# Performance work log

Hardware: AMD Instinct MI355X
Metric: run time of the kernel (lower is better)

## Reference

```python
import jax, jax.numpy as jnp
import numpy as np

H = 512      # hidden_size
N = 8        # num_heads (each head has full H dims in this module)
B, T = 4, 1024
LN_EPS = 1e-5


def _layernorm(x, gamma, beta):
    mu = jnp.mean(x, axis=-1, keepdims=True)
    var = jnp.mean(jnp.square(x - mu), axis=-1, keepdims=True)
    return (x - mu) * jax.lax.rsqrt(var + LN_EPS) * gamma + beta


def setup_inputs() -> dict:
    key = jax.random.key(0)
    ks = jax.random.split(key, 8)
    s = 0.02
    return {
        "x":   jax.random.normal(ks[0], (B, T, H), dtype=jnp.float32),
        "Wq":  jax.random.normal(ks[1], (H, N * H), dtype=jnp.float32) * s,
        "Wk":  jax.random.normal(ks[2], (H, N * H), dtype=jnp.float32) * s,
        "Wv":  jax.random.normal(ks[3], (H, N * H), dtype=jnp.float32) * s,
        "Wo":  jax.random.normal(ks[4], (N * H, H), dtype=jnp.float32) * s,
        "g1":  jnp.ones((H,), jnp.float32),
        "beta1": jnp.zeros((H,), jnp.float32),
        "Wf1": jax.random.normal(ks[5], (H, 4 * H), dtype=jnp.float32) * s,
        "bf1": jnp.zeros((4 * H,), jnp.float32),
        "Wf2": jax.random.normal(ks[6], (4 * H, H), dtype=jnp.float32) * s,
        "bf2": jnp.zeros((H,), jnp.float32),
        "g2":  jnp.ones((H,), jnp.float32),
        "beta2": jnp.zeros((H,), jnp.float32),
    }


def reference(x, Wq, Wk, Wv, Wo, g1, beta1, Wf1, bf1, Wf2, bf2, g2, beta2):
    b, t, h = x.shape
    n = Wq.shape[1] // h
    # torch .view(B, N, T, H) on a contiguous (B, T, N*H) tensor is a raw
    # row-major reshape (NOT a transpose) -> identical to jnp.reshape.
    Q = (x @ Wq).reshape(b, n, t, h)
    K = (x @ Wk).reshape(b, n, t, h)
    V = (x @ Wv).reshape(b, n, t, h)
    # 'bath,bahT->batT' with K.transpose(2,3) == standard Q @ K^T per (b,a)
    logits = jnp.einsum('bath,baTh->batT', Q, K)
    attn = jax.nn.softmax(logits / (h ** 0.5), axis=-1)
    # repeated 't' in one operand takes the DIAGONAL of attn (torch semantics,
    # matched by numpy/jax einsum): h[b,a,t,:] = attn[b,a,t,t] * V[b,a,t,:]
    hh = jnp.einsum('batt,bath->bath', attn, V)
    hh = hh.reshape(b, t, n * h) @ Wo
    hh = _layernorm(x + hh, g1, beta1)
    ff = jax.nn.relu(hh @ Wf1 + bf1) @ Wf2 + bf2
    return _layernorm(hh + ff, g2, beta2)
```

## Files before the change

### kernel.cpp

```cpp
#include <hip/hip_runtime.h>
#include <stdint.h>


#define LN_EPS 1e-5f

typedef __attribute__((ext_vector_type(8))) short short8;
typedef __attribute__((ext_vector_type(4))) float f32x4;
typedef __attribute__((ext_vector_type(4))) int int4v;

__device__ __forceinline__ unsigned short f2bf(float f) {
    unsigned int u = __float_as_uint(f);
    u = (u + 0x7fffu + ((u >> 16) & 1u)) >> 16;
    return (unsigned short)u;
}
__device__ __forceinline__ float bf2f(unsigned short h) {
    return __uint_as_float(((unsigned int)h) << 16);
}
__device__ __forceinline__ signed char q8(float v, float s) {
    int q = (int)rintf(v * s);
    q = q > 127 ? 127 : (q < -127 ? -127 : q);
    return (signed char)q;
}
__device__ __forceinline__ int pperm(int w) {
    return (w & ~63) + ((w & 15) << 2) + ((w >> 4) & 3);
}

__device__ __forceinline__ void llds16(const void* g, void* l) {
    __builtin_amdgcn_global_load_lds(
        (const __attribute__((address_space(1))) void*)g,
        (__attribute__((address_space(3))) void*)l, 16, 0, 0);
}

__global__ __launch_bounds__(256) void prep(
    const float* __restrict__ Wq, const float* __restrict__ Wk,
    const float* __restrict__ Wv, unsigned short* __restrict__ Wqb,
    const float* __restrict__ x, signed char* __restrict__ xq,
    const float* __restrict__ Wo, unsigned short* __restrict__ WoT,
    const float* __restrict__ Wf1, signed char* __restrict__ Wf1Tq,
    const float* __restrict__ Wf2, signed char* __restrict__ Wf2Tq,
    float* __restrict__ dsum) {
    __shared__ float tile[32][33];
    const int bid = blockIdx.x;
    const int tid = threadIdx.x;

    if (bid < 3072) {
        const int y = bid >> 10;
        const int idx = (bid & 1023) * 256 + tid;
        const float* src = (y == 0) ? Wq : (y == 1) ? Wk : Wv;
        float4 a = ((const float4*)src)[idx * 2];
        float4 b = ((const float4*)src)[idx * 2 + 1];
        uint4 o;
        o.x = (unsigned int)f2bf(a.x) | ((unsigned int)f2bf(a.y) << 16);
        o.y = (unsigned int)f2bf(a.z) | ((unsigned int)f2bf(a.w) << 16);
        o.z = (unsigned int)f2bf(b.x) | ((unsigned int)f2bf(b.y) << 16);
        o.w = (unsigned int)f2bf(b.z) | ((unsigned int)f2bf(b.w) << 16);
        ((uint4*)(Wqb + (long)y * 2097152))[idx] = o;
    } else if (bid < 5120) {
        const int idx = (bid - 3072) * 256 + tid;
        const int t = idx >> 7;
        const int rem = idx & 127;
        const int g = rem >> 4, lr = rem & 15;
        const long rb = (long)t * 512 + g * 64;
        unsigned int o = 0;
#pragma unroll
        for (int n = 0; n < 4; ++n)
            o |= (unsigned int)(unsigned char)q8(x[rb + n * 16 + lr], 32.f)
                 << (8 * n);
        *(unsigned int*)(xq + rb + lr * 4) = o;
    } else if (bid < 7168) {
        const int r = bid - 5120;
        const int bx = r & 15, by = r >> 4;
        const int tx = tid & 31, ty = tid >> 5;
        const int r0 = by * 32, c0 = bx * 32;
        const int R = 4096, C = 512;
#pragma unroll
        for (int k = 0; k < 4; ++k)
            tile[ty + k * 8][tx] =
                Wo[(long)(r0 + ty + k * 8) * C + c0 + tx];
        __syncthreads();
#pragma unroll
        for (int k = 0; k < 4; ++k)
            WoT[(long)(c0 + ty + k * 8) * R + r0 + tx] =
                f2bf(tile[tx][ty + k * 8]);
    } else if (bid < 8192) {
        const int r = bid - 7168;
        const int bx = r & 63, by = r >> 6;
        const int tx = tid & 31, ty = tid >> 5;
        const int r0 = by * 32, c0 = bx * 32;
        const int R = 512, C = 2048;
#pragma unroll
        for (int k = 0; k < 4; ++k)
            tile[ty + k * 8][tx] =
                Wf1[(long)(r0 + ty + k * 8) * C + c0 + tx];
        __syncthreads();
#pragma unroll
        for (int k = 0; k < 4; ++k)
            Wf1Tq[(long)(c0 + ty + k * 8) * R + (r0 + tx)] =
                q8(tile[tx][ty + k * 8], 1024.f);
    } else if (bid < 9216) {
        const int r = bid - 8192;
        const int bx = r & 15, by = r >> 4;
        const int tx = tid & 31, ty = tid >> 5;
        const int r0 = by * 32, c0 = bx * 32;
        const int R = 2048, C = 512;
#pragma unroll
        for (int k = 0; k < 4; ++k)
            tile[ty + k * 8][tx] =
                Wf2[(long)(r0 + ty + k * 8) * C + c0 + tx];
        __syncthreads();
#pragma unroll
        for (int k = 0; k < 4; ++k) {
            const int rr = r0 + tx;
            Wf2Tq[(long)(c0 + ty + k * 8) * R + pperm(rr)] =
                q8(tile[tx][ty + k * 8], 1024.f);
        }
    } else {
        const int idx = (bid - 9216) * 256 + tid;
        dsum[idx] = 0.f;
    }
}

__global__ __launch_bounds__(256) void gemm_fold(
    const unsigned short* __restrict__ A,
    const unsigned short* __restrict__ Bt,
    const unsigned short* __restrict__ A2,
    const unsigned short* __restrict__ B2,
    signed char* __restrict__ Cv,
    int N, int K, int lda, int ldb,
    long aBatch, long bBatch, long cBatch) {
    __shared__ unsigned short As[128 * 64];
    __shared__ unsigned short Bs[128 * 64];

    const int bx = blockIdx.x, by = blockIdx.y, bz = blockIdx.z;
    const int tid = threadIdx.x;
    const int wid = tid >> 6;
    const int lane = tid & 63;
    const int lr = lane & 15;
    const int kg = lane >> 4;
    const int wr = wid >> 1;
    const int wc = wid & 1;
    const int row0 = by * 128;
    const int col0 = bx * 128;

    const int zf = bz >> 3, za = bz & 7;
    const unsigned short* Ab = (zf ? A2 : A) + (long)za * aBatch;
    const unsigned short* Bb = (zf ? B2 : Bt) + (long)za * bBatch;
    const long cOff = (long)bz * cBatch;

    const int l8 = lane >> 3;
    const int cs = ((lane & 7) ^ l8) * 8;
    unsigned short* ldsA = &As[wid * 2048];
    unsigned short* ldsB = &Bs[wid * 2048];
    const unsigned short* gA = Ab + (long)(row0 + wid * 32 + l8) * lda + cs;
    const unsigned short* gB = Bb + (long)(col0 + wid * 32 + l8) * ldb + cs;

    const int lr7 = lr & 7;
    const int uS0 = ((0 + kg) ^ lr7) * 8;
    const int uS1 = ((4 + kg) ^ lr7) * 8;

    f32x4 acc[4][4];
#pragma unroll
    for (int m = 0; m < 4; ++m)
#pragma unroll
        for (int n = 0; n < 4; ++n)
#pragma unroll
            for (int j = 0; j < 4; ++j) acc[m][n][j] = 0.f;

    for (int kk = 0; kk < K; kk += 64) {
        __syncthreads();
#pragma unroll
        for (int i = 0; i < 4; ++i) {
            llds16(gA + (long)i * 8 * lda + kk, ldsA + i * 512);
            llds16(gB + (long)i * 8 * ldb + kk, ldsB + i * 512);
        }
        __syncthreads();
        short8 a[4][2], b[4][2];
#pragma unroll
        for (int m = 0; m < 4; ++m) {
            const int ro = (wr * 64 + m * 16 + lr) * 64;
            a[m][0] = *(const short8*)&As[ro + uS0];
            a[m][1] = *(const short8*)&As[ro + uS1];
        }
#pragma unroll
        for (int n = 0; n < 4; ++n) {
            const int ro = (wc * 64 + n * 16 + lr) * 64;
            b[n][0] = *(const short8*)&Bs[ro + uS0];
            b[n][1] = *(const short8*)&Bs[ro + uS1];
        }
#pragma unroll
        for (int s = 0; s < 2; ++s)
#pragma unroll
            for (int m = 0; m < 4; ++m)
#pragma unroll
                for (int n = 0; n < 4; ++n)
                    acc[m][n] = __builtin_amdgcn_mfma_f32_16x16x32_bf16(
                        a[m][s], b[n][s], acc[m][n], 0, 0, 0);
    }

    const int gbase = col0 + wc * 64 + lr * 4;
#pragma unroll
    for (int m = 0; m < 4; ++m) {
        const int grow = row0 + wr * 64 + m * 16 + kg * 4;
#pragma unroll
        for (int j = 0; j < 4; ++j) {
            unsigned int o = 0;
#pragma unroll
            for (int n = 0; n < 4; ++n)
                o |= (unsigned int)(unsigned char)q8(acc[m][n][j], 2048.f)
                     << (8 * n);
            *(unsigned int*)(Cv + cOff + (long)(grow + j) * N + gbase) = o;
        }
    }
}

template <int IM>
__global__ __launch_bounds__(256) void gemm_i8(
    const signed char* __restrict__ Abase,
    const signed char* __restrict__ Bbase,
    signed char* __restrict__ o8,
    unsigned short* __restrict__ o16,
    const float* __restrict__ bias,
    float* __restrict__ dsum, float* __restrict__ ddiag,
    float invs2048) {
    __shared__ signed char As[128 * 128];
    __shared__ signed char Bs[128 * 128];

    const unsigned gx = gridDim.x, gy = gridDim.y;
    const unsigned nwg = gx * gy * gridDim.z;
    unsigned flat = blockIdx.x + gx * (blockIdx.y + gy * blockIdx.z);
    flat = (flat & 7u) * (nwg >> 3) + (flat >> 3);
    const int bx = flat % gx;
    const int by = (flat / gx) % gy;
    const int bz = flat / (gx * gy);

    const int tid = threadIdx.x;
    const int wid = tid >> 6;
    const int lane = tid & 63;
    const int lr = lane & 15;
    const int kg = lane >> 4;
    const int wr = wid >> 1;
    const int wc = wid & 1;
    const int row0 = by * 128;
    const int col0 = bx * 128;

    int lda, ldb, k0 = 0;
    const signed char* Ab;
    const signed char* Bb;
    if (IM == 0) {
        lda = 512; ldb = 512;
        Ab = Abase;
        Bb = Bbase + (long)bz * (4096 * 512);
    } else if (IM == 1) {
        lda = 4096; ldb = 512;
        const int b = bz >> 3, a = bz & 7;
        Ab = Abase + (long)b * (1024 * 4096) + a * 512;
        Bb = Bbase + (long)b * (1024 * 512);
    } else if (IM == 2) {
        lda = 512; ldb = 512;
        Ab = Abase; Bb = Bbase;
    } else {
        lda = 2048; ldb = 2048;
        Ab = Abase; Bb = Bbase;
        k0 = bz * 512;
    }

    const int l8 = lane >> 3;
    const int cs = ((lane & 7) ^ l8) * 16;
    signed char* ldsA = &As[wid * 4096];
    signed char* ldsB = &Bs[wid * 4096];
    const signed char* gA = Ab + (long)(row0 + wid * 32 + l8) * lda + k0 + cs;
    const signed char* gB = Bb + (long)(col0 + wid * 32 + l8) * ldb + k0 + cs;

    const int lr7 = lr & 7;
    const int uS0 = ((0 + kg) ^ lr7) * 16;
    const int uS1 = ((4 + kg) ^ lr7) * 16;

    int4v acc[4][4];
#pragma unroll
    for (int m = 0; m < 4; ++m)
#pragma unroll
        for (int n = 0; n < 4; ++n)
#pragma unroll
            for (int j = 0; j < 4; ++j) acc[m][n][j] = 0;

    for (int kt = 0; kt < 4; ++kt) {
        const int kk = kt * 128;
        __syncthreads();
#pragma unroll
        for (int i = 0; i < 4; ++i) {
            llds16(gA + (long)i * 8 * lda + kk, ldsA + i * 1024);
            llds16(gB + (long)i * 8 * ldb + kk, ldsB + i * 1024);
        }
        __syncthreads();
        int4v av[4][2], bv[4][2];
#pragma unroll
        for (int m = 0; m < 4; ++m) {
            const int ro = (wr * 64 + m * 16 + lr) * 128;
            av[m][0] = *(const int4v*)&As[ro + uS0];
            av[m][1] = *(const int4v*)&As[ro + uS1];
        }
#pragma unroll
        for (int n = 0; n < 4; ++n) {
            const int ro = (wc * 64 + n * 16 + lr) * 128;
            bv[n][0] = *(const int4v*)&Bs[ro + uS0];
            bv[n][1] = *(const int4v*)&Bs[ro + uS1];
        }
#pragma unroll
        for (int s = 0; s < 2; ++s)
#pragma unroll
            for (int m = 0; m < 4; ++m)
#pragma unroll
                for (int n = 0; n < 4; ++n)
                    acc[m][n] = __builtin_amdgcn_mfma_i32_16x16x64_i8(
                        av[m][s], bv[n][s], acc[m][n], 0, 0, 0);
    }

    if (IM == 1) {
        const float dq = 1.52587890625e-5f;
        const int hrow0 = bz * 1024 + row0 + wr * 64;
        const bool diagblk = (bx == by) && (wr == wc);
#pragma unroll
        for (int m = 0; m < 4; ++m) {
            float es[4] = {0.f, 0.f, 0.f, 0.f};
#pragma unroll
            for (int n = 0; n < 4; ++n) {
#pragma unroll
                for (int j = 0; j < 4; ++j) {
                    const float e = __expf((float)acc[m][n][j] * dq);
                    es[j] += e;
                    if (diagblk && n == m && lr == kg * 4 + j)
                        ddiag[hrow0 + m * 16 + kg * 4 + j] = e;
                }
            }
#pragma unroll
            for (int j = 0; j < 4; ++j) {
                float s = es[j];
                s += __shfl_xor(s, 1, 64);
                s += __shfl_xor(s, 2, 64);
                s += __shfl_xor(s, 4, 64);
                s += __shfl_xor(s, 8, 64);
                if (lr == 0) atomicAdd(&dsum[hrow0 + m * 16 + kg * 4 + j], s);
            }
        }
        return;
    }

    const int gbase = col0 + wc * 64 + lr * 4;
#pragma unroll
    for (int m = 0; m < 4; ++m) {
        const int grow = row0 + wr * 64 + m * 16 + kg * 4;
#pragma unroll
        for (int j = 0; j < 4; ++j) {
            if (IM == 0) {
                unsigned int o = 0;
                const float s = (bz == 0) ? invs2048 : 128.f;
#pragma unroll
                for (int n = 0; n < 4; ++n) {
                    const float v = (float)acc[m][n][j] * 1.52587890625e-5f;
                    o |= (unsigned int)(unsigned char)q8(v, s) << (8 * n);
                }
                const long off = (bz == 0) ? 0 : (long)16777216;
                *(unsigned int*)(o8 + off + (long)(grow + j) * 4096 + gbase) = o;
            } else if (IM == 2) {
                unsigned int o = 0;
#pragma unroll
                for (int n = 0; n < 4; ++n) {
                    const int ocol = col0 + wc * 64 + n * 16 + lr;
                    const float v = fmaxf(
                        fmaf((float)acc[m][n][j], 3.0517578125e-5f,
                             bias[ocol]), 0.f);
                    o |= (unsigned int)(unsigned char)q8(v, 64.f) << (8 * n);
                }
                *(unsigned int*)(o8 + (long)(grow + j) * 2048 + gbase) = o;
            } else {
                const float v0 = (float)acc[m][0][j] * 1.52587890625e-5f;
                const float v1 = (float)acc[m][1][j] * 1.52587890625e-5f;
                const float v2 = (float)acc[m][2][j] * 1.52587890625e-5f;
                const float v3 = (float)acc[m][3][j] * 1.52587890625e-5f;
                uint2 o;
                o.x = (unsigned int)f2bf(v0) | ((unsigned int)f2bf(v1) << 16);
                o.y = (unsigned int)f2bf(v2) | ((unsigned int)f2bf(v3) << 16);
                *(uint2*)(o16 + (long)bz * 2097152 + (long)(grow + j) * 512 +
                          gbase) = o;
            }
        }
    }
}

__device__ __forceinline__ void ln_reduce(float v0, float v1, int tid,
                                          float* sred, float* sred2,
                                          float& mu, float& rs) {
    float sum = v0 + v1;
    float sq = v0 * v0 + v1 * v1;
#pragma unroll
    for (int off = 32; off > 0; off >>= 1) {
        sum += __shfl_down(sum, off, 64);
        sq += __shfl_down(sq, off, 64);
    }
    const int wave = tid >> 6;
    if ((tid & 63) == 0) { sred[wave] = sum; sred2[wave] = sq; }
    __syncthreads();
    if (tid == 0) {
        float s = 0.f, q = 0.f;
#pragma unroll
        for (int w = 0; w < 4; ++w) { s += sred[w]; q += sred2[w]; }
        const float m = s * (1.f / 512.f);
        const float var = q * (1.f / 512.f) - m * m;
        sred[4] = m;
        sred2[4] = rsqrtf(var + LN_EPS);
    }
    __syncthreads();
    mu = sred[4];
    rs = sred2[4];
}

__global__ __launch_bounds__(256) void ln_combine1(
    const float* __restrict__ x, const signed char* __restrict__ Uq,
    const float* __restrict__ dsum, const float* __restrict__ ddiag,
    const float* __restrict__ g, const float* __restrict__ be,
    float* __restrict__ y1, signed char* __restrict__ y1q) {
    __shared__ float sred[8], sred2[8], df[8];
    const int row = blockIdx.x;
    const int tid = threadIdx.x;
    if (tid < 8) {
        const int b = row >> 10, t = row & 1023;
        const int idx = (b * 8 + tid) * 1024 + t;
        df[tid] = ddiag[idx] / dsum[idx] * (1.f / 128.f);
    }
    __syncthreads();
    const long base = (long)row * 512;
    const long ubase = (long)row * 4096;
    const int p0 = pperm(tid);
    const int p1 = pperm(tid + 256);
    float v0 = x[base + tid];
    float v1 = x[base + tid + 256];
#pragma unroll
    for (int a = 0; a < 8; ++a) {
        const float d = df[a];
        const long ub = ubase + a * 512;
        v0 = fmaf(d, (float)Uq[ub + p0], v0);
        v1 = fmaf(d, (float)Uq[ub + p1], v1);
    }
    float mu, rs;
    ln_reduce(v0, v1, tid, sred, sred2, mu, rs);
    const float o0 = (v0 - mu) * rs * g[tid] + be[tid];
    const float o1 = (v1 - mu) * rs * g[tid + 256] + be[tid + 256];
    y1[base + tid] = o0;
    y1[base + tid + 256] = o1;
    y1q[base + tid] = q8(o0, 32.f);
    y1q[base + tid + 256] = q8(o1, 32.f);
}

__global__ __launch_bounds__(256) void ln_combine2(
    const float* __restrict__ y1, const unsigned short* __restrict__ ffp,
    const float* __restrict__ bias, const float* __restrict__ g,
    const float* __restrict__ be, float* __restrict__ out) {
    __shared__ float sred[8], sred2[8];
    const int row = blockIdx.x;
    const int tid = threadIdx.x;
    const long base = (long)row * 512;
    const int p0 = pperm(tid);
    const int p1 = pperm(tid + 256);
    float v0 = y1[base + tid] + bias[tid];
    float v1 = y1[base + tid + 256] + bias[tid + 256];
#pragma unroll
    for (int z = 0; z < 4; ++z) {
        const long fb = (long)z * 2097152 + base;
        v0 += bf2f(ffp[fb + p0]);
        v1 += bf2f(ffp[fb + p1]);
    }
    float mu, rs;
    ln_reduce(v0, v1, tid, sred, sred2, mu, rs);
    out[base + tid] = (v0 - mu) * rs * g[tid] + be[tid];
    out[base + tid + 256] = (v1 - mu) * rs * g[tid + 256] + be[tid + 256];
}

extern "C" void kernel_launch(void* const* d_in, const int* in_sizes, int n_in,
                              void* d_out, int out_size, void* d_ws, size_t ws_size,
                              hipStream_t stream) {
    const float* x     = (const float*)d_in[0];
    const float* Wq    = (const float*)d_in[1];
    const float* Wk    = (const float*)d_in[2];
    const float* Wv    = (const float*)d_in[3];
    const float* Wo    = (const float*)d_in[4];
    const float* g1    = (const float*)d_in[5];
    const float* beta1 = (const float*)d_in[6];
    const float* Wf1   = (const float*)d_in[7];
    const float* bf1   = (const float*)d_in[8];
    const float* Wf2   = (const float*)d_in[9];
    const float* bf2   = (const float*)d_in[10];
    const float* g2    = (const float*)d_in[11];
    const float* beta2 = (const float*)d_in[12];
    float* out = (float*)d_out;

    char* p = (char*)d_ws;
    unsigned short* Wqb  = (unsigned short*)p; p += (long)512 * 4096 * 2;
    unsigned short* Wkb  = (unsigned short*)p; p += (long)512 * 4096 * 2;
    unsigned short* Wvb  = (unsigned short*)p; p += (long)512 * 4096 * 2;
    unsigned short* WoT  = (unsigned short*)p; p += (long)512 * 4096 * 2;
    signed char*  Wf1Tq  = (signed char*)p;    p += (long)2048 * 512;
    signed char*  Wf2Tq  = (signed char*)p;    p += (long)512 * 2048;
    signed char*  Wallq8 = (signed char*)p;    p += (long)8192 * 512;
    signed char*  PUq8   = (signed char*)p;    p += (long)2 * 4096 * 4096;
    signed char*  xq8    = (signed char*)p;    p += (long)4096 * 512;
    signed char*  y1q8   = (signed char*)p;    p += (long)4096 * 512;
    signed char*  f1q8   = (signed char*)p;    p += (long)4096 * 2048;
    float* dsum  = (float*)p; p += (long)32768 * 4;
    float* ddiag = (float*)p; p += (long)32768 * 4;
    float* y1    = (float*)p; p += (long)4096 * 512 * 4;
    unsigned short* ffp = (unsigned short*)p; p += (long)4 * 4096 * 512 * 2;

    const dim3 blk(256);
    const float invs = 0.04419417382415922f;

    prep<<<dim3(9344), blk, 0, stream>>>(Wq, Wk, Wv, Wqb, x, xq8, Wo, WoT,
                                         Wf1, Wf1Tq, Wf2, Wf2Tq, dsum);

    gemm_fold<<<dim3(4, 4, 16), blk, 0, stream>>>(
        Wkb, Wqb, WoT, Wvb, Wallq8,
        512, 512, 4096, 4096, 512, 512, (long)512 * 512);

    gemm_i8<0><<<dim3(32, 32, 2), blk, 0, stream>>>(
        xq8, Wallq8, PUq8, nullptr, nullptr, nullptr, nullptr, invs * 2048.f);

    gemm_i8<1><<<dim3(8, 8, 32), blk, 0, stream>>>(
        PUq8, xq8, nullptr, nullptr, nullptr, dsum, ddiag, 0.f);

    ln_combine1<<<dim3(4096), blk, 0, stream>>>(
        x, PUq8 + (long)16777216, dsum, ddiag, g1, beta1, y1, y1q8);

    gemm_i8<2><<<dim3(16, 32, 1), blk, 0, stream>>>(
        y1q8, Wf1Tq, f1q8, nullptr, bf1, nullptr, nullptr, 0.f);

    gemm_i8<3><<<dim3(4, 32, 4), blk, 0, stream>>>(
        f1q8, Wf2Tq, nullptr, ffp, nullptr, nullptr, nullptr, 0.f);

    ln_combine2<<<dim3(4096), blk, 0, stream>>>(y1, ffp, bf2, g2, beta2, out);
}
```

Before: 124.2 us.

## Keep B panel resident in LDS across four row tiles for int8 GEMMs

Adds a gemm_pers kernel for the two large int8 GEMMs (projection and attention-logit). Each block loads its 128x512 B column panel into dynamic LDS once and loops over four consecutive row tiles, streaming only A tiles. This cuts repeated B global loads and launches a quarter as many blocks. In exchange it needs 80KB of LDS per block, which lowers occupancy, and the per-k-step loop is not double-buffered.

```diff
diff --git a/kernel.cpp b/kernel.cpp
--- a/kernel.cpp
+++ b/kernel.cpp
@@ -75,8 +75,7 @@
         const int R = 4096, C = 512;
 #pragma unroll
         for (int k = 0; k < 4; ++k)
-            tile[ty + k * 8][tx] =
-                Wo[(long)(r0 + ty + k * 8) * C + c0 + tx];
+            tile[ty + k * 8][tx] = Wo[(long)(r0 + ty + k * 8) * C + c0 + tx];
         __syncthreads();
 #pragma unroll
         for (int k = 0; k < 4; ++k)
@@ -90,8 +89,7 @@
         const int R = 512, C = 2048;
 #pragma unroll
         for (int k = 0; k < 4; ++k)
-            tile[ty + k * 8][tx] =
-                Wf1[(long)(r0 + ty + k * 8) * C + c0 + tx];
+            tile[ty + k * 8][tx] = Wf1[(long)(r0 + ty + k * 8) * C + c0 + tx];
         __syncthreads();
 #pragma unroll
         for (int k = 0; k < 4; ++k)
@@ -105,8 +103,7 @@
         const int R = 2048, C = 512;
 #pragma unroll
         for (int k = 0; k < 4; ++k)
-            tile[ty + k * 8][tx] =
-                Wf2[(long)(r0 + ty + k * 8) * C + c0 + tx];
+            tile[ty + k * 8][tx] = Wf2[(long)(r0 + ty + k * 8) * C + c0 + tx];
         __syncthreads();
 #pragma unroll
         for (int k = 0; k < 4; ++k) {
@@ -214,14 +211,176 @@
 }
 
 template <int IM>
+__global__ __launch_bounds__(256) void gemm_pers(
+    const signed char* __restrict__ Abase,
+    const signed char* __restrict__ Bbase,
+    signed char* __restrict__ o8,
+    float* __restrict__ dsum, float* __restrict__ ddiag,
+    float invs2048) {
+    extern __shared__ signed char lds[];
+    signed char* Bs = lds;
+    signed char* As = lds + 65536;
+
+    const unsigned gx = gridDim.x, gy = gridDim.y;
+    const unsigned nwg = gx * gy * gridDim.z;
+    unsigned flat = blockIdx.x + gx * (blockIdx.y + gy * blockIdx.z);
+    flat = (flat & 7u) * (nwg >> 3) + (flat >> 3);
+    const int bx = flat % gx;
+    const int byh = (flat / gx) % gy;
+    const int bz = flat / (gx * gy);
+
+    const int tid = threadIdx.x;
+    const int wid = tid >> 6;
+    const int lane = tid & 63;
+    const int lr = lane & 15;
+    const int kg = lane >> 4;
+    const int wr = wid >> 1;
+    const int wc = wid & 1;
+    const int col0 = bx * 128;
+
+    int lda;
+    const signed char* Ab;
+    const signed char* Bb;
+    if (IM == 0) {
+        lda = 512;
+        Ab = Abase;
+        Bb = Bbase + (long)bz * (4096 * 512) + (long)col0 * 512;
+    } else {
+        lda = 4096;
+        const int b = bz >> 3, a = bz & 7;
+        Ab = Abase + (long)b * (1024 * 4096) + a * 512;
+        Bb = Bbase + (long)b * (1024 * 512) + (long)col0 * 512;
+    }
+
+    {
+        const int l5 = lane >> 5;
+        const int u5 = lane & 31;
+        const int ktS = u5 >> 3, u3 = u5 & 7;
+#pragma unroll
+        for (int i = 0; i < 16; ++i) {
+            const int r = wid * 32 + i * 2 + l5;
+            const signed char* g =
+                Bb + (long)r * 512 + ktS * 128 + ((u3 ^ (r & 7)) * 16);
+            llds16(g, Bs + (wid * 32 + i * 2) * 512);
+        }
+    }
+
+    const int l8 = lane >> 3;
+    const int cs = ((lane & 7) ^ l8) * 16;
+    signed char* ldsA = As + wid * 4096;
+
+    const int lr7 = lr & 7;
+    const int uS0 = ((0 + kg) ^ lr7) * 16;
+    const int uS1 = ((4 + kg) ^ lr7) * 16;
+
+    const int nby = (IM == 0) ? 32 : 8;
+    (void)nby;
+
+#pragma unroll 1
+    for (int byl = 0; byl < 4; ++byl) {
+        const int by = byh * 4 + byl;
+        const int row0 = by * 128;
+        const signed char* gA =
+            Ab + (long)(row0 + wid * 32 + l8) * lda + cs;
+
+        int4v acc[4][4];
+#pragma unroll
+        for (int m = 0; m < 4; ++m)
+#pragma unroll
+            for (int n = 0; n < 4; ++n)
+#pragma unroll
+                for (int j = 0; j < 4; ++j) acc[m][n][j] = 0;
+
+#pragma unroll 1
+        for (int kt = 0; kt < 4; ++kt) {
+            const int kk = kt * 128;
+#pragma unroll
+            for (int i = 0; i < 4; ++i)
+                llds16(gA + (long)i * 8 * lda + kk, ldsA + i * 1024);
+            __syncthreads();
+            int4v av[4][2], bv[4][2];
+#pragma unroll
+            for (int m = 0; m < 4; ++m) {
+                const int ro = (wr * 64 + m * 16 + lr) * 128;
+                av[m][0] = *(const int4v*)&As[ro + uS0];
+                av[m][1] = *(const int4v*)&As[ro + uS1];
+            }
+#pragma unroll
+            for (int n = 0; n < 4; ++n) {
+                const int ro = (wc * 64 + n * 16 + lr) * 512 + kk;
+                bv[n][0] = *(const int4v*)&Bs[ro + uS0];
+                bv[n][1] = *(const int4v*)&Bs[ro + uS1];
+            }
+#pragma unroll
+            for (int s = 0; s < 2; ++s)
+#pragma unroll
+                for (int m = 0; m < 4; ++m)
+#pragma unroll
+                    for (int n = 0; n < 4; ++n)
+                        acc[m][n] = __builtin_amdgcn_mfma_i32_16x16x64_i8(
+                            av[m][s], bv[n][s], acc[m][n], 0, 0, 0);
+            __syncthreads();
+        }
+
+        if (IM == 1) {
+            const float dq = 1.52587890625e-5f;
+            const int hrow0 = bz * 1024 + row0 + wr * 64;
+            const bool diagblk = (bx == by) && (wr == wc);
+#pragma unroll
+            for (int m = 0; m < 4; ++m) {
+                float es[4] = {0.f, 0.f, 0.f, 0.f};
+#pragma unroll
+                for (int n = 0; n < 4; ++n) {
+#pragma unroll
+                    for (int j = 0; j < 4; ++j) {
+                        const float e = __expf((float)acc[m][n][j] * dq);
+                        es[j] += e;
+                        if (diagblk && n == m && lr == kg * 4 + j)
+                            ddiag[hrow0 + m * 16 + kg * 4 + j] = e;
+                    }
+                }
+#pragma unroll
+                for (int j = 0; j < 4; ++j) {
+                    float s = es[j];
+                    s += __shfl_xor(s, 1, 64);
+                    s += __shfl_xor(s, 2, 64);
+                    s += __shfl_xor(s, 4, 64);
+                    s += __shfl_xor(s, 8, 64);
+                    if (lr == 0)
+                        atomicAdd(&dsum[hrow0 + m * 16 + kg * 4 + j], s);
+                }
+            }
+        } else {
+            const int gbase = col0 + wc * 64 + lr * 4;
+            const float s = (bz == 0) ? invs2048 : 128.f;
+            const long off = (bz == 0) ? 0 : (long)16777216;
+#pragma unroll
+            for (int m = 0; m < 4; ++m) {
+                const int grow = row0 + wr * 64 + m * 16 + kg * 4;
+#pragma unroll
+                for (int j = 0; j < 4; ++j) {
+                    unsigned int o = 0;
+#pragma unroll
+                    for (int n = 0; n < 4; ++n) {
+                        const float v =
+                            (float)acc[m][n][j] * 1.52587890625e-5f;
+                        o |= (unsigned int)(unsigned char)q8(v, s) << (8 * n);
+                    }
+                    *(unsigned int*)(o8 + off + (long)(grow + j) * 4096 +
+                                     gbase) = o;
+                }
+            }
+        }
+    }
+}
+
+template <int IM>
 __global__ __launch_bounds__(256) void gemm_i8(
     const signed char* __restrict__ Abase,
     const signed char* __restrict__ Bbase,
     signed char* __restrict__ o8,
     unsigned short* __restrict__ o16,
-    const float* __restrict__ bias,
-    float* __restrict__ dsum, float* __restrict__ ddiag,
-    float invs2048) {
+    const float* __restrict__ bias) {
     __shared__ signed char As[128 * 128];
     __shared__ signed char Bs[128 * 128];
 
@@ -244,23 +403,12 @@
     const int col0 = bx * 128;
 
     int lda, ldb, k0 = 0;
-    const signed char* Ab;
-    const signed char* Bb;
-    if (IM == 0) {
+    const signed char* Ab = Abase;
+    const signed char* Bb = Bbase;
+    if (IM == 2) {
         lda = 512; ldb = 512;
-        Ab = Abase;
-        Bb = Bbase + (long)bz * (4096 * 512);
-    } else if (IM == 1) {
-        lda = 4096; ldb = 512;
-        const int b = bz >> 3, a = bz & 7;
-        Ab = Abase + (long)b * (1024 * 4096) + a * 512;
-        Bb = Bbase + (long)b * (1024 * 512);
-    } else if (IM == 2) {
-        lda = 512; ldb = 512;
-        Ab = Abase; Bb = Bbase;
     } else {
         lda = 2048; ldb = 2048;
-        Ab = Abase; Bb = Bbase;
         k0 = bz * 512;
     }
 
@@ -315,53 +463,13 @@
                         av[m][s], bv[n][s], acc[m][n], 0, 0, 0);
     }
 
-    if (IM == 1) {
-        const float dq = 1.52587890625e-5f;
-        const int hrow0 = bz * 1024 + row0 + wr * 64;
-        const bool diagblk = (bx == by) && (wr == wc);
-#pragma unroll
-        for (int m = 0; m < 4; ++m) {
-            float es[4] = {0.f, 0.f, 0.f, 0.f};
-#pragma unroll
-            for (int n = 0; n < 4; ++n) {
-#pragma unroll
-                for (int j = 0; j < 4; ++j) {
-                    const float e = __expf((float)acc[m][n][j] * dq);
-                    es[j] += e;
-                    if (diagblk && n == m && lr == kg * 4 + j)
-                        ddiag[hrow0 + m * 16 + kg * 4 + j] = e;
-                }
-            }
-#pragma unroll
-            for (int j = 0; j < 4; ++j) {
-                float s = es[j];
-                s += __shfl_xor(s, 1, 64);
-                s += __shfl_xor(s, 2, 64);
-                s += __shfl_xor(s, 4, 64);
-                s += __shfl_xor(s, 8, 64);
-                if (lr == 0) atomicAdd(&dsum[hrow0 + m * 16 + kg * 4 + j], s);
-            }
-        }
-        return;
-    }
-
     const int gbase = col0 + wc * 64 + lr * 4;
 #pragma unroll
     for (int m = 0; m < 4; ++m) {
         const int grow = row0 + wr * 64 + m * 16 + kg * 4;
 #pragma unroll
         for (int j = 0; j < 4; ++j) {
-            if (IM == 0) {
-                unsigned int o = 0;
-                const float s = (bz == 0) ? invs2048 : 128.f;
-#pragma unroll
-                for (int n = 0; n < 4; ++n) {
-                    const float v = (float)acc[m][n][j] * 1.52587890625e-5f;
-                    o |= (unsigned int)(unsigned char)q8(v, s) << (8 * n);
-                }
-                const long off = (bz == 0) ? 0 : (long)16777216;
-                *(unsigned int*)(o8 + off + (long)(grow + j) * 4096 + gbase) = o;
-            } else if (IM == 2) {
+            if (IM == 2) {
                 unsigned int o = 0;
 #pragma unroll
                 for (int n = 0; n < 4; ++n) {
@@ -512,6 +620,12 @@
 
     const dim3 blk(256);
     const float invs = 0.04419417382415922f;
+    const int PLDS = 81920;
+
+    hipFuncSetAttribute(reinterpret_cast<const void*>(&gemm_pers<0>),
+                        hipFuncAttributeMaxDynamicSharedMemorySize, PLDS);
+    hipFuncSetAttribute(reinterpret_cast<const void*>(&gemm_pers<1>),
+                        hipFuncAttributeMaxDynamicSharedMemorySize, PLDS);
 
     prep<<<dim3(9344), blk, 0, stream>>>(Wq, Wk, Wv, Wqb, x, xq8, Wo, WoT,
                                          Wf1, Wf1Tq, Wf2, Wf2Tq, dsum);
@@ -520,20 +634,20 @@
         Wkb, Wqb, WoT, Wvb, Wallq8,
         512, 512, 4096, 4096, 512, 512, (long)512 * 512);
 
-    gemm_i8<0><<<dim3(32, 32, 2), blk, 0, stream>>>(
-        xq8, Wallq8, PUq8, nullptr, nullptr, nullptr, nullptr, invs * 2048.f);
-
-    gemm_i8<1><<<dim3(8, 8, 32), blk, 0, stream>>>(
-        PUq8, xq8, nullptr, nullptr, nullptr, dsum, ddiag, 0.f);
+    gemm_pers<0><<<dim3(32, 8, 2), blk, PLDS, stream>>>(
+        xq8, Wallq8, PUq8, nullptr, nullptr, invs * 2048.f);
+
+    gemm_pers<1><<<dim3(8, 2, 32), blk, PLDS, stream>>>(
+        PUq8, xq8, nullptr, dsum, ddiag, 0.f);
 
     ln_combine1<<<dim3(4096), blk, 0, stream>>>(
         x, PUq8 + (long)16777216, dsum, ddiag, g1, beta1, y1, y1q8);
 
     gemm_i8<2><<<dim3(16, 32, 1), blk, 0, stream>>>(
-        y1q8, Wf1Tq, f1q8, nullptr, bf1, nullptr, nullptr, 0.f);
+        y1q8, Wf1Tq, f1q8, nullptr, bf1);
 
     gemm_i8<3><<<dim3(4, 32, 4), blk, 0, stream>>>(
-        f1q8, Wf2Tq, nullptr, ffp, nullptr, nullptr, nullptr, 0.f);
+        f1q8, Wf2Tq, nullptr, ffp, nullptr);
 
     ln_combine2<<<dim3(4096), blk, 0, stream>>>(y1, ffp, bf2, g2, beta2, out);
 }
```

New measurement: 127.9 us. 1.03x slower.
